# Kernel tuning notes

Hardware: AMD Instinct MI355X
Metric: run time of the kernel (lower is better)

Reference implementation:

```python
import jax, jax.numpy as jnp
import numpy as np

B, N, NEMBED, E, H = 4, 256, 10000, 63, 128
D = E + 1  # feature dim after concat = 64


def _lin(key, fan_in, fan_out):
    k1, k2 = jax.random.split(key)
    bound = 1.0 / np.sqrt(fan_in)
    W = jax.random.uniform(k1, (fan_in, fan_out), jnp.float32, -bound, bound)
    b = jax.random.uniform(k2, (fan_out,), jnp.float32, -bound, bound)
    return W, b


def setup_inputs() -> dict:
    key = jax.random.key(0)
    ks = jax.random.split(key, 9)
    xcat = jax.random.randint(ks[0], (B, N), 0, NEMBED, dtype=jnp.int64)
    xfeat = jax.random.normal(ks[1], (B, N), dtype=jnp.float32)
    emb = jax.random.normal(ks[2], (NEMBED, E), dtype=jnp.float32)
    W1, b1 = _lin(ks[3], D, H)
    W2, b2 = _lin(ks[4], H, H)
    W3, b3 = _lin(ks[5], H, H)
    D1, c1 = _lin(ks[6], H, H)
    D2, c2 = _lin(ks[7], H, H)
    D3, c3 = _lin(ks[8], H, 1)
    return {"xcat": xcat, "xfeat": xfeat, "emb": emb,
            "W1": W1, "b1": b1, "W2": W2, "b2": b2, "W3": W3, "b3": b3,
            "D1": D1, "c1": c1, "D2": D2, "c2": c2, "D3": D3, "c3": c3}


def reference(xcat, xfeat, emb, W1, b1, W2, b2, W3, b3, D1, c1, D2, c2, D3, c3):
    # embed + concat scalar feature -> [B, N, D]
    x = jnp.concatenate([emb[xcat], xfeat[..., None]], axis=-1)
    # pairwise outer product over the set dim -> [B, N, N, D]
    # (original: einsum 'bid,bjd->bdij' then permute(0,2,3,1) == 'bid,bjd->bijd')
    p = jnp.einsum('bid,bjd->bijd', x, x)
    # per-pair 3-layer MLP (enc)
    h = jnp.maximum(p @ W1 + b1, 0.0)
    h = jnp.maximum(h @ W2 + b2, 0.0)
    h = h @ W3 + b3
    # relu -> mean pool over (i, j) -> relu; dropout is identity in eval
    h = jnp.maximum(h, 0.0)
    h = jnp.mean(h, axis=(1, 2))  # [B, H]
    h = jnp.maximum(h, 0.0)
    # dec MLP -> [B, 1]
    h = jnp.maximum(h @ D1 + c1, 0.0)
    h = jnp.maximum(h @ D2 + c2, 0.0)
    return h @ D3 + c3
```

## Files before the change

### kernel.cpp

```cpp
#include <hip/hip_runtime.h>
#include <hip/hip_bf16.h>


#define NB 4
#define NN 256
#define HD 128
#define BPB 65
#define NPAIR 32896

typedef __attribute__((ext_vector_type(8))) short bf16x8;
typedef __attribute__((ext_vector_type(4))) float f32x4;

__device__ __forceinline__ unsigned rne2(float a, float b) {
    unsigned ua = __builtin_bit_cast(unsigned, a);
    unsigned ub = __builtin_bit_cast(unsigned, b);
    ua = ua + 0x7fff + ((ua >> 16) & 1);
    ub = ub + 0x7fff + ((ub >> 16) & 1);
    return (ua >> 16) | (ub & 0xffff0000u);
}

__device__ __forceinline__ short f2bf(float f) {
    unsigned u = __builtin_bit_cast(unsigned, f);
    u = (u + 0x7fff + ((u >> 16) & 1)) >> 16;
    return (short)u;
}

__device__ __forceinline__ void tri_ij(int t, int& i, int& j) {
    j = (int)((sqrtf(8.0f * (float)t + 1.0f) - 1.0f) * 0.5f);
    while (((j + 1) * (j + 2) >> 1) <= t) ++j;
    while (((j * (j + 1)) >> 1) > t) --j;
    i = t - ((j * (j + 1)) >> 1);
}

__device__ __forceinline__ void pack_w_nat(const float* __restrict__ W, short* __restrict__ pw,
                                           int KQ, int u) {
    int l  = u & 63;
    int kq = (u >> 6) % KQ;
    int mt = (u >> 6) / KQ;
    int q = l >> 4, m = l & 15;
    int c = mt * 16 + m;
#pragma unroll
    for (int j = 0; j < 8; ++j) {
        int k = kq * 32 + q * 8 + j;
        pw[u * 8 + j] = f2bf(W[k * 128 + c]);
    }
}

__device__ __forceinline__ void pack_w_perm(const float* __restrict__ W, short* __restrict__ pw,
                                            int u) {
    int l  = u & 63;
    int kq = (u >> 6) & 3;
    int mt = (u >> 6) >> 2;
    int q = l >> 4, m = l & 15;
    int c = mt * 16 + m;
#pragma unroll
    for (int j = 0; j < 8; ++j) {
        int k = 32 * kq + 16 * (j >> 2) + 4 * q + (j & 3);
        pw[u * 8 + j] = f2bf(W[k * 128 + c]);
    }
}

__global__ void prep_kernel(const int* __restrict__ xcat,
                            const float* __restrict__ xfeat,
                            const float* __restrict__ emb,
                            const float* __restrict__ W1,
                            const float* __restrict__ W2,
                            const float* __restrict__ W3,
                            float* __restrict__ x,
                            short* __restrict__ pw1,
                            short* __restrict__ pw2,
                            short* __restrict__ pw3)
{
    int bid = blockIdx.x;
    int tid = threadIdx.x;
    if (bid < 256) {
        int f = bid * 256 + tid;
        int d = f & 63;
        int nn = f >> 6;
        float v;
        if (d < 63) v = emb[xcat[nn] * 63 + d];
        else        v = xfeat[nn];
        x[f] = v;
    } else if (bid < 260) {
        pack_w_nat(W1, pw1, 2, (bid - 256) * 256 + tid);
    } else if (bid < 268) {
        pack_w_perm(W2, pw2, (bid - 260) * 256 + tid);
    } else {
        pack_w_perm(W3, pw3, (bid - 268) * 256 + tid);
    }
}

__global__ __launch_bounds__(512, 2) void pair_mlp(
    const float* __restrict__ x,
    const short* __restrict__ pw1g, const float* __restrict__ b1,
    const short* __restrict__ pw2g, const float* __restrict__ b2,
    const short* __restrict__ pw3g, const float* __restrict__ b3,
    float* __restrict__ partialOut)
{
    __shared__ __align__(16) short smW[32768];

    const int tid = threadIdx.x;
    const int w = __builtin_amdgcn_readfirstlane(tid >> 6);
    const int l = tid & 63;
    const int q = l >> 4;
    const int n = l & 15;
    const int b = blockIdx.y;
    const float* xb = x + (b << 14);

    float4* H0w = (float4*)smW;
    float4* H1w = (float4*)(smW + 16384);
    const float4* s1 = (const float4*)pw1g;
    const float4* s2 = (const float4*)pw2g;
    const float4* s3 = (const float4*)pw3g;
    float4 g3[4];
    {
        float4 g1a = s1[tid], g1b = s1[tid + 512];
        float4 g2[4];
#pragma unroll
        for (int k = 0; k < 4; ++k) g2[k] = s2[tid + 512 * k];
#pragma unroll
        for (int k = 0; k < 4; ++k) g3[k] = s3[tid + 512 * k];
        H0w[tid] = g1a; H0w[tid + 512] = g1b;
#pragma unroll
        for (int k = 0; k < 4; ++k) H1w[tid + 512 * k] = g2[k];
    }

    const int base = blockIdx.x * 512 + w * 64 + n;
    int iv[4], jv[4];
    float wp[4];
#pragma unroll
    for (int nt = 0; nt < 4; ++nt) {
        int praw = base + nt * 16;
        int pc = praw <= (NPAIR - 1) ? praw : (NPAIR - 1);
        tri_ij(pc, iv[nt], jv[nt]);
        wp[nt] = (praw <= (NPAIR - 1)) ? ((iv[nt] == jv[nt]) ? 1.0f : 2.0f) : 0.0f;
    }

    bf16x8 bp[4][2];
#pragma unroll
    for (int nt = 0; nt < 4; ++nt) {
        const float* xi = xb + (iv[nt] << 6);
        const float* xj = xb + (jv[nt] << 6);
#pragma unroll
        for (int kq = 0; kq < 2; ++kq) {
            int dd = kq * 32 + q * 8;
            float4 A0 = *(const float4*)(xi + dd);
            float4 A1 = *(const float4*)(xi + dd + 4);
            float4 B0 = *(const float4*)(xj + dd);
            float4 B1 = *(const float4*)(xj + dd + 4);
            uint4 s;
            s.x = rne2(A0.x * B0.x, A0.y * B0.y);
            s.y = rne2(A0.z * B0.z, A0.w * B0.w);
            s.z = rne2(A1.x * B1.x, A1.y * B1.y);
            s.w = rne2(A1.z * B1.z, A1.w * B1.w);
            bp[nt][kq] = __builtin_bit_cast(bf16x8, s);
        }
    }
    __syncthreads();

    const bf16x8* F0 = (const bf16x8*)smW;
    const bf16x8* F1 = (const bf16x8*)(smW + 16384);

    f32x4 acc[8][4];
    unsigned pk[4][8][2];

#pragma unroll
    for (int mt = 0; mt < 8; ++mt) {
        float4 bv = *(const float4*)(b1 + mt * 16 + q * 4);
        f32x4 init = {bv.x, bv.y, bv.z, bv.w};
#pragma unroll
        for (int nt = 0; nt < 4; ++nt) acc[mt][nt] = init;
    }
#pragma unroll
    for (int kq = 0; kq < 2; ++kq)
#pragma unroll
        for (int mt = 0; mt < 8; ++mt) {
            bf16x8 afr = F0[(mt * 2 + kq) * 64 + l];
#pragma unroll
            for (int nt = 0; nt < 4; ++nt)
                acc[mt][nt] = __builtin_amdgcn_mfma_f32_16x16x32_bf16(afr, bp[nt][kq], acc[mt][nt], 0, 0, 0);
        }

#pragma unroll
    for (int nt = 0; nt < 4; ++nt)
#pragma unroll
        for (int mt = 0; mt < 8; ++mt) {
            pk[nt][mt][0] = rne2(fmaxf(acc[mt][nt][0], 0.f), fmaxf(acc[mt][nt][1], 0.f));
            pk[nt][mt][1] = rne2(fmaxf(acc[mt][nt][2], 0.f), fmaxf(acc[mt][nt][3], 0.f));
        }

    __syncthreads();
    H0w[tid] = g3[0]; H0w[tid + 512] = g3[1];
    H0w[tid + 1024] = g3[2]; H0w[tid + 1536] = g3[3];

#pragma unroll
    for (int mt = 0; mt < 8; ++mt) {
        float4 bv = *(const float4*)(b2 + mt * 16 + q * 4);
        f32x4 init = {bv.x, bv.y, bv.z, bv.w};
#pragma unroll
        for (int nt = 0; nt < 4; ++nt) acc[mt][nt] = init;
    }
#pragma unroll
    for (int kq = 0; kq < 4; ++kq) {
        bf16x8 bf[4];
#pragma unroll
        for (int nt = 0; nt < 4; ++nt) {
            uint4 u = {pk[nt][2 * kq][0], pk[nt][2 * kq][1],
                       pk[nt][2 * kq + 1][0], pk[nt][2 * kq + 1][1]};
            bf[nt] = __builtin_bit_cast(bf16x8, u);
        }
#pragma unroll
        for (int mt = 0; mt < 8; ++mt) {
            bf16x8 afr = F1[(mt * 4 + kq) * 64 + l];
#pragma unroll
            for (int nt = 0; nt < 4; ++nt)
                acc[mt][nt] = __builtin_amdgcn_mfma_f32_16x16x32_bf16(afr, bf[nt], acc[mt][nt], 0, 0, 0);
        }
    }

#pragma unroll
    for (int nt = 0; nt < 4; ++nt)
#pragma unroll
        for (int mt = 0; mt < 8; ++mt) {
            pk[nt][mt][0] = rne2(fmaxf(acc[mt][nt][0], 0.f), fmaxf(acc[mt][nt][1], 0.f));
            pk[nt][mt][1] = rne2(fmaxf(acc[mt][nt][2], 0.f), fmaxf(acc[mt][nt][3], 0.f));
        }

    __syncthreads();

#pragma unroll
    for (int mt = 0; mt < 8; ++mt) {
        float4 bv = *(const float4*)(b3 + mt * 16 + q * 4);
        f32x4 init = {bv.x, bv.y, bv.z, bv.w};
#pragma unroll
        for (int nt = 0; nt < 4; ++nt) acc[mt][nt] = init;
    }
#pragma unroll
    for (int kq = 0; kq < 4; ++kq) {
        bf16x8 bf[4];
#pragma unroll
        for (int nt = 0; nt < 4; ++nt) {
            uint4 u = {pk[nt][2 * kq][0], pk[nt][2 * kq][1],
                       pk[nt][2 * kq + 1][0], pk[nt][2 * kq + 1][1]};
            bf[nt] = __builtin_bit_cast(bf16x8, u);
        }
#pragma unroll
        for (int mt = 0; mt < 8; ++mt) {
            bf16x8 afr = F0[(mt * 4 + kq) * 64 + l];
#pragma unroll
            for (int nt = 0; nt < 4; ++nt)
                acc[mt][nt] = __builtin_amdgcn_mfma_f32_16x16x32_bf16(afr, bf[nt], acc[mt][nt], 0, 0, 0);
        }
    }

    const int row = (b * BPB + blockIdx.x) * 8 + w;
#pragma unroll
    for (int mt = 0; mt < 8; ++mt) {
        float vs[4];
#pragma unroll
        for (int r = 0; r < 4; ++r) {
            float v = wp[0] * fmaxf(acc[mt][0][r], 0.f) + wp[1] * fmaxf(acc[mt][1][r], 0.f)
                    + wp[2] * fmaxf(acc[mt][2][r], 0.f) + wp[3] * fmaxf(acc[mt][3][r], 0.f);
            v += __shfl_xor(v, 1, 64);
            v += __shfl_xor(v, 2, 64);
            v += __shfl_xor(v, 4, 64);
            v += __shfl_xor(v, 8, 64);
            vs[r] = v;
        }
        if (n == 0) {
            float4 o = {vs[0], vs[1], vs[2], vs[3]};
            *(float4*)(partialOut + row * HD + mt * 16 + q * 4) = o;
        }
    }
}

#define RROWS (BPB * 8)
__global__ __launch_bounds__(1024) void reduce_decode(
    const float* __restrict__ partial,
    const float* __restrict__ D1, const float* __restrict__ c1,
    const float* __restrict__ D2, const float* __restrict__ c2,
    const float* __restrict__ D3, const float* __restrict__ c3,
    float* __restrict__ out)
{
    __shared__ float red8[8][HD];
    __shared__ float red2[2][HD];
    __shared__ float hb[HD];
    __shared__ float tb[HD];
    const int b = blockIdx.x;
    const int t = threadIdx.x;
    const int ch = t & 127, sl = t >> 7;

    {
        const float* base = partial + b * RROWS * HD + ch;
        float s0 = 0.f, s1 = 0.f, s2 = 0.f, s3 = 0.f;
        int tl = sl;
        for (; tl + 32 <= RROWS; tl += 32) {
            s0 += base[(tl     ) * HD];
            s1 += base[(tl +  8) * HD];
            s2 += base[(tl + 16) * HD];
            s3 += base[(tl + 24) * HD];
        }
        for (; tl < RROWS; tl += 8) s0 += base[tl * HD];
        red8[sl][ch] = (s0 + s1) + (s2 + s3);
    }
    __syncthreads();
    if (sl == 0) {
        float v = ((red8[0][ch] + red8[1][ch]) + (red8[2][ch] + red8[3][ch]))
                + ((red8[4][ch] + red8[5][ch]) + (red8[6][ch] + red8[7][ch]));
        hb[ch] = fmaxf(v * (1.0f / 65536.0f), 0.0f);
    }
    __syncthreads();

    const int hf = sl & 1;

    if (t < 256) {
        float a = 0.f;
        for (int k = hf * 64; k < hf * 64 + 64; ++k)
            a = fmaf(hb[k], D1[(k << 7) + ch], a);
        red2[hf][ch] = a;
    }
    __syncthreads();
    if (t < 128)
        tb[ch] = fmaxf(red2[0][ch] + red2[1][ch] + c1[ch], 0.0f);
    __syncthreads();

    if (t < 256) {
        float a = 0.f;
        for (int k = hf * 64; k < hf * 64 + 64; ++k)
            a = fmaf(tb[k], D2[(k << 7) + ch], a);
        red2[hf][ch] = a;
    }
    __syncthreads();
    if (t < 128)
        hb[ch] = fmaxf(red2[0][ch] + red2[1][ch] + c2[ch], 0.0f);
    __syncthreads();

    if (t < 128) red2[0][ch] = hb[ch] * D3[ch];
    __syncthreads();
    if (t < 64) {
        float r = red2[0][t] + red2[0][t + 64];
#pragma unroll
        for (int s2 = 1; s2 < 64; s2 <<= 1)
            r += __shfl_xor(r, s2, 64);
        if (t == 0) out[b] = r + c3[0];
    }
}

extern "C" void kernel_launch(void* const* d_in, const int* in_sizes, int n_in,
                              void* d_out, int out_size, void* d_ws, size_t ws_size,
                              hipStream_t stream)
{
    (void)in_sizes; (void)n_in; (void)out_size; (void)ws_size;

    const int*   xcat  = (const int*)  d_in[0];
    const float* xfeat = (const float*)d_in[1];
    const float* emb   = (const float*)d_in[2];
    const float* W1    = (const float*)d_in[3];
    const float* b1    = (const float*)d_in[4];
    const float* W2    = (const float*)d_in[5];
    const float* b2    = (const float*)d_in[6];
    const float* W3    = (const float*)d_in[7];
    const float* b3    = (const float*)d_in[8];
    const float* D1    = (const float*)d_in[9];
    const float* c1    = (const float*)d_in[10];
    const float* D2    = (const float*)d_in[11];
    const float* c2    = (const float*)d_in[12];
    const float* D3    = (const float*)d_in[13];
    const float* c3    = (const float*)d_in[14];
    float* out = (float*)d_out;

    float* x       = (float*)d_ws;
    short* pw1     = (short*)(x + NB * NN * 64);
    short* pw2     = pw1 + 8 * 2 * 64 * 8;
    short* pw3     = pw2 + 8 * 4 * 64 * 8;
    float* partial = (float*)(pw3 + 8 * 4 * 64 * 8);

    prep_kernel<<<276, 256, 0, stream>>>(xcat, xfeat, emb, W1, W2, W3,
                                         x, pw1, pw2, pw3);
    pair_mlp<<<dim3(BPB, NB), 512, 0, stream>>>(x, pw1, b1, pw2, b2, pw3, b3, partial);
    reduce_decode<<<NB, 1024, 0, stream>>>(partial, D1, c1, D2, c2, D3, c3, out);
}
```

Before: 131.0 us.

## Halve pairs per block, double grid, reduce warp partials in shared memory

Each block now handles 256 pairs instead of 512 (two 16-pair tiles per wave instead of four), so the grid per batch roughly doubles to 129 blocks. The launch-bounds occupancy hint drops from 2 to 1. Per-wave partial sums are now reduced across the 8 waves in shared memory before one row per block is written, which shrinks the partial buffer and the reduce kernel's work. Weight stores to LDS are moved after the x loads. The intent is more parallelism across CUs and less global partial traffic, at the cost of loading the weights twice as often per pair and getting less MFMA work per weight fragment read.

Result: no change. 129.0 us (-1.6%).

```diff
diff --git a/kernel.cpp b/kernel.cpp
--- a/kernel.cpp
+++ b/kernel.cpp
@@ -5,7 +5,7 @@
 #define NB 4
 #define NN 256
 #define HD 128
-#define BPB 65
+#define BPB 129
 #define NPAIR 32896
 
 typedef __attribute__((ext_vector_type(8))) short bf16x8;
@@ -90,7 +90,7 @@
     }
 }
 
-__global__ __launch_bounds__(512, 2) void pair_mlp(
+__global__ __launch_bounds__(512, 1) void pair_mlp(
     const float* __restrict__ x,
     const short* __restrict__ pw1g, const float* __restrict__ b1,
     const short* __restrict__ pw2g, const float* __restrict__ b2,
@@ -112,33 +112,28 @@
     const float4* s1 = (const float4*)pw1g;
     const float4* s2 = (const float4*)pw2g;
     const float4* s3 = (const float4*)pw3g;
-    float4 g3[4];
-    {
-        float4 g1a = s1[tid], g1b = s1[tid + 512];
-        float4 g2[4];
-#pragma unroll
-        for (int k = 0; k < 4; ++k) g2[k] = s2[tid + 512 * k];
-#pragma unroll
-        for (int k = 0; k < 4; ++k) g3[k] = s3[tid + 512 * k];
-        H0w[tid] = g1a; H0w[tid + 512] = g1b;
-#pragma unroll
-        for (int k = 0; k < 4; ++k) H1w[tid + 512 * k] = g2[k];
-    }
-
-    const int base = blockIdx.x * 512 + w * 64 + n;
-    int iv[4], jv[4];
-    float wp[4];
-#pragma unroll
-    for (int nt = 0; nt < 4; ++nt) {
+
+    float4 g1a = s1[tid], g1b = s1[tid + 512];
+    float4 g2[4], g3[4];
+#pragma unroll
+    for (int k = 0; k < 4; ++k) g2[k] = s2[tid + 512 * k];
+#pragma unroll
+    for (int k = 0; k < 4; ++k) g3[k] = s3[tid + 512 * k];
+
+    const int base = blockIdx.x * 256 + w * 32 + n;
+    int iv[2], jv[2];
+    float wp[2];
+#pragma unroll
+    for (int nt = 0; nt < 2; ++nt) {
         int praw = base + nt * 16;
         int pc = praw <= (NPAIR - 1) ? praw : (NPAIR - 1);
         tri_ij(pc, iv[nt], jv[nt]);
         wp[nt] = (praw <= (NPAIR - 1)) ? ((iv[nt] == jv[nt]) ? 1.0f : 2.0f) : 0.0f;
     }
 
-    bf16x8 bp[4][2];
-#pragma unroll
-    for (int nt = 0; nt < 4; ++nt) {
+    bf16x8 bp[2][2];
+#pragma unroll
+    for (int nt = 0; nt < 2; ++nt) {
         const float* xi = xb + (iv[nt] << 6);
         const float* xj = xb + (jv[nt] << 6);
 #pragma unroll
@@ -156,33 +151,35 @@
             bp[nt][kq] = __builtin_bit_cast(bf16x8, s);
         }
     }
+
+    H0w[tid] = g1a; H0w[tid + 512] = g1b;
+#pragma unroll
+    for (int k = 0; k < 4; ++k) H1w[tid + 512 * k] = g2[k];
     __syncthreads();
 
     const bf16x8* F0 = (const bf16x8*)smW;
     const bf16x8* F1 = (const bf16x8*)(smW + 16384);
 
-    f32x4 acc[8][4];
-    unsigned pk[4][8][2];
+    f32x4 acc[8][2];
+    unsigned pk[2][8][2];
 
 #pragma unroll
     for (int mt = 0; mt < 8; ++mt) {
         float4 bv = *(const float4*)(b1 + mt * 16 + q * 4);
         f32x4 init = {bv.x, bv.y, bv.z, bv.w};
-#pragma unroll
-        for (int nt = 0; nt < 4; ++nt) acc[mt][nt] = init;
+        acc[mt][0] = init; acc[mt][1] = init;
     }
 #pragma unroll
     for (int kq = 0; kq < 2; ++kq)
 #pragma unroll
         for (int mt = 0; mt < 8; ++mt) {
             bf16x8 afr = F0[(mt * 2 + kq) * 64 + l];
-#pragma unroll
-            for (int nt = 0; nt < 4; ++nt)
-                acc[mt][nt] = __builtin_amdgcn_mfma_f32_16x16x32_bf16(afr, bp[nt][kq], acc[mt][nt], 0, 0, 0);
-        }
-
-#pragma unroll
-    for (int nt = 0; nt < 4; ++nt)
+            acc[mt][0] = __builtin_amdgcn_mfma_f32_16x16x32_bf16(afr, bp[0][kq], acc[mt][0], 0, 0, 0);
+            acc[mt][1] = __builtin_amdgcn_mfma_f32_16x16x32_bf16(afr, bp[1][kq], acc[mt][1], 0, 0, 0);
+        }
+
+#pragma unroll
+    for (int nt = 0; nt < 2; ++nt)
 #pragma unroll
         for (int mt = 0; mt < 8; ++mt) {
             pk[nt][mt][0] = rne2(fmaxf(acc[mt][nt][0], 0.f), fmaxf(acc[mt][nt][1], 0.f));
@@ -197,14 +194,13 @@
     for (int mt = 0; mt < 8; ++mt) {
         float4 bv = *(const float4*)(b2 + mt * 16 + q * 4);
         f32x4 init = {bv.x, bv.y, bv.z, bv.w};
-#pragma unroll
-        for (int nt = 0; nt < 4; ++nt) acc[mt][nt] = init;
+        acc[mt][0] = init; acc[mt][1] = init;
     }
 #pragma unroll
     for (int kq = 0; kq < 4; ++kq) {
-        bf16x8 bf[4];
-#pragma unroll
-        for (int nt = 0; nt < 4; ++nt) {
+        bf16x8 bf[2];
+#pragma unroll
+        for (int nt = 0; nt < 2; ++nt) {
             uint4 u = {pk[nt][2 * kq][0], pk[nt][2 * kq][1],
                        pk[nt][2 * kq + 1][0], pk[nt][2 * kq + 1][1]};
             bf[nt] = __builtin_bit_cast(bf16x8, u);
@@ -212,14 +208,13 @@
 #pragma unroll
         for (int mt = 0; mt < 8; ++mt) {
             bf16x8 afr = F1[(mt * 4 + kq) * 64 + l];
-#pragma unroll
-            for (int nt = 0; nt < 4; ++nt)
-                acc[mt][nt] = __builtin_amdgcn_mfma_f32_16x16x32_bf16(afr, bf[nt], acc[mt][nt], 0, 0, 0);
-        }
-    }
-
-#pragma unroll
-    for (int nt = 0; nt < 4; ++nt)
+            acc[mt][0] = __builtin_amdgcn_mfma_f32_16x16x32_bf16(afr, bf[0], acc[mt][0], 0, 0, 0);
+            acc[mt][1] = __builtin_amdgcn_mfma_f32_16x16x32_bf16(afr, bf[1], acc[mt][1], 0, 0, 0);
+        }
+    }
+
+#pragma unroll
+    for (int nt = 0; nt < 2; ++nt)
 #pragma unroll
         for (int mt = 0; mt < 8; ++mt) {
             pk[nt][mt][0] = rne2(fmaxf(acc[mt][nt][0], 0.f), fmaxf(acc[mt][nt][1], 0.f));
@@ -232,14 +227,13 @@
     for (int mt = 0; mt < 8; ++mt) {
         float4 bv = *(const float4*)(b3 + mt * 16 + q * 4);
         f32x4 init = {bv.x, bv.y, bv.z, bv.w};
-#pragma unroll
-        for (int nt = 0; nt < 4; ++nt) acc[mt][nt] = init;
+        acc[mt][0] = init; acc[mt][1] = init;
     }
 #pragma unroll
     for (int kq = 0; kq < 4; ++kq) {
-        bf16x8 bf[4];
-#pragma unroll
-        for (int nt = 0; nt < 4; ++nt) {
+        bf16x8 bf[2];
+#pragma unroll
+        for (int nt = 0; nt < 2; ++nt) {
             uint4 u = {pk[nt][2 * kq][0], pk[nt][2 * kq][1],
                        pk[nt][2 * kq + 1][0], pk[nt][2 * kq + 1][1]};
             bf[nt] = __builtin_bit_cast(bf16x8, u);
@@ -247,20 +241,18 @@
 #pragma unroll
         for (int mt = 0; mt < 8; ++mt) {
             bf16x8 afr = F0[(mt * 4 + kq) * 64 + l];
-#pragma unroll
-            for (int nt = 0; nt < 4; ++nt)
-                acc[mt][nt] = __builtin_amdgcn_mfma_f32_16x16x32_bf16(afr, bf[nt], acc[mt][nt], 0, 0, 0);
-        }
-    }
-
-    const int row = (b * BPB + blockIdx.x) * 8 + w;
+            acc[mt][0] = __builtin_amdgcn_mfma_f32_16x16x32_bf16(afr, bf[0], acc[mt][0], 0, 0, 0);
+            acc[mt][1] = __builtin_amdgcn_mfma_f32_16x16x32_bf16(afr, bf[1], acc[mt][1], 0, 0, 0);
+        }
+    }
+
+    float* smPart = (float*)(smW + 16384);
 #pragma unroll
     for (int mt = 0; mt < 8; ++mt) {
         float vs[4];
 #pragma unroll
         for (int r = 0; r < 4; ++r) {
-            float v = wp[0] * fmaxf(acc[mt][0][r], 0.f) + wp[1] * fmaxf(acc[mt][1][r], 0.f)
-                    + wp[2] * fmaxf(acc[mt][2][r], 0.f) + wp[3] * fmaxf(acc[mt][3][r], 0.f);
+            float v = wp[0] * fmaxf(acc[mt][0][r], 0.f) + wp[1] * fmaxf(acc[mt][1][r], 0.f);
             v += __shfl_xor(v, 1, 64);
             v += __shfl_xor(v, 2, 64);
             v += __shfl_xor(v, 4, 64);
@@ -269,12 +261,19 @@
         }
         if (n == 0) {
             float4 o = {vs[0], vs[1], vs[2], vs[3]};
-            *(float4*)(partialOut + row * HD + mt * 16 + q * 4) = o;
-        }
-    }
-}
-
-#define RROWS (BPB * 8)
+            *(float4*)(smPart + w * HD + mt * 16 + q * 4) = o;
+        }
+    }
+    __syncthreads();
+
+    if (tid < HD) {
+        float v = 0.f;
+#pragma unroll
+        for (int ww = 0; ww < 8; ++ww) v += smPart[ww * HD + tid];
+        partialOut[(b * BPB + blockIdx.x) * HD + tid] = v;
+    }
+}
+
 __global__ __launch_bounds__(1024) void reduce_decode(
     const float* __restrict__ partial,
     const float* __restrict__ D1, const float* __restrict__ c1,
@@ -291,16 +290,16 @@
     const int ch = t & 127, sl = t >> 7;
 
     {
-        const float* base = partial + b * RROWS * HD + ch;
+        const float* base = partial + b * BPB * HD + ch;
         float s0 = 0.f, s1 = 0.f, s2 = 0.f, s3 = 0.f;
         int tl = sl;
-        for (; tl + 32 <= RROWS; tl += 32) {
+        for (; tl + 32 <= BPB; tl += 32) {
             s0 += base[(tl     ) * HD];
             s1 += base[(tl +  8) * HD];
             s2 += base[(tl + 16) * HD];
             s3 += base[(tl + 24) * HD];
         }
-        for (; tl < RROWS; tl += 8) s0 += base[tl * HD];
+        for (; tl < BPB; tl += 8) s0 += base[tl * HD];
         red8[sl][ch] = (s0 + s1) + (s2 + s3);
     }
     __syncthreads();
```
